# Performance work log

Hardware: AMD Instinct MI355X
Metric: run time of the kernel (lower is better)

## Reference

```python
import jax, jax.numpy as jnp
import numpy as np

N_NODES = 100000
N_EDGES = 600000
N_GRAPHS = 64
EPS = 1e-5


def setup_inputs() -> dict:
    key = jax.random.key(0)
    ks = jax.random.split(key, 8)
    x = jax.random.normal(ks[0], (N_NODES, 128), dtype=jnp.float32)
    edge_index = jax.random.randint(ks[1], (2, N_EDGES), 0, N_NODES, dtype=jnp.int64)
    batch = jnp.sort(jax.random.randint(ks[2], (N_NODES,), 0, N_GRAPHS, dtype=jnp.int64))
    conv_w = jax.random.normal(ks[3], (6, 128, 128), dtype=jnp.float32) * (1.0 / np.sqrt(128))
    conv_b = jnp.zeros((6, 128), dtype=jnp.float32)
    bn_g = jnp.ones((6, 128), dtype=jnp.float32)
    bn_b = jnp.zeros((6, 128), dtype=jnp.float32)
    lin1_w = jax.random.normal(ks[4], (128, 64), dtype=jnp.float32) * (1.0 / np.sqrt(128))
    lin1_b = jnp.zeros((64,), dtype=jnp.float32)
    lin2_w = jax.random.normal(ks[5], (64, 4), dtype=jnp.float32) * (1.0 / np.sqrt(64))
    lin2_b = jnp.zeros((4,), dtype=jnp.float32)
    return {"x": x, "edge_index": edge_index, "batch": batch,
            "conv_w": conv_w, "conv_b": conv_b, "bn_g": bn_g, "bn_b": bn_b,
            "lin1_w": lin1_w, "lin1_b": lin1_b, "lin2_w": lin2_w, "lin2_b": lin2_b}


def reference(x, edge_index, batch, conv_w, conv_b, bn_g, bn_b, lin1_w, lin1_b, lin2_w, lin2_b):
    src, dst = edge_index[0], edge_index[1]  # messages flow src -> dst (PyG source_to_target)
    n = x.shape[0]
    h = x
    # 6 stacked GCNConv(normalize=False) -> ReLU -> BatchNorm1d (training-mode batch stats)
    for i in range(6):
        m = h @ conv_w[i]                                   # [N, H] transform first
        agg = jax.ops.segment_sum(m[src], dst, num_segments=n) + conv_b[i]
        h = jax.nn.relu(agg)
        mean = h.mean(axis=0)
        var = h.var(axis=0)                                  # biased, matches torch BN
        h = (h - mean) * jax.lax.rsqrt(var + EPS) * bn_g[i] + bn_b[i]
    # global mean pool over graphs
    s = jax.ops.segment_sum(h, batch, num_segments=N_GRAPHS)          # [G, H]
    cnt = jax.ops.segment_sum(jnp.ones((n,), h.dtype), batch, num_segments=N_GRAPHS)
    pooled = s / jnp.maximum(cnt, 1.0)[:, None]
    out = pooled @ lin1_w + lin1_b
    out = out @ lin2_w + lin2_b
    return jax.nn.log_softmax(out, axis=-1)
```

## Files before the change

kernel.cpp:

```cpp
#include <hip/hip_runtime.h>
#include <math.h>

#define NN 100000
#define NE 600000
#define NG 64
#define HD 128
#define NL 6
#define NB 1563
#define PSL 16
#define ASTR 136
#define CASTB 12500

typedef unsigned short ushort_t;
typedef short short8 __attribute__((ext_vector_type(8)));
typedef float floatx4 __attribute__((ext_vector_type(4)));

__device__ __forceinline__ float bf2f(ushort_t u) {
    return __uint_as_float(((unsigned)u) << 16);
}
__device__ __forceinline__ ushort_t f2bf(float f) {
    unsigned u = __float_as_uint(f);
    unsigned r = (u + 0x7fffu + ((u >> 16) & 1u)) >> 16;
    return (ushort_t)r;
}


__global__ __launch_bounds__(256) void k_prep(const float* __restrict__ x,
                                              ushort_t* __restrict__ xb,
                                              const float* __restrict__ W,
                                              ushort_t* __restrict__ Wt,
                                              ushort_t* __restrict__ hb0,
                                              ushort_t* __restrict__ hb1) {
    if (blockIdx.x < CASTB) {
        int i = blockIdx.x * 256 + threadIdx.x;
        float4 v = ((const float4*)x)[i];
        ((ushort4*)xb)[i] = make_ushort4(f2bf(v.x), f2bf(v.y), f2bf(v.z), f2bf(v.w));
    } else {
        const float* Wl = W + (size_t)(blockIdx.x - CASTB) * 16384;
        ushort_t* Wtl = Wt + (size_t)(blockIdx.x - CASTB) * 16384;
        for (int id = threadIdx.x; id < 16384; id += 256) {
            int k = id >> 7, c = id & 127;
            Wtl[c * 128 + k] = f2bf(Wl[id]);
        }
        if (blockIdx.x == CASTB && threadIdx.x < 96) {
            int t = threadIdx.x;
            ushort_t* base = (t < 32) ? xb : ((t < 64) ? hb0 : hb1);
            *(ushort4*)(base + (size_t)NN * 128 + (size_t)(t & 31) * 4) =
                make_ushort4(0, 0, 0, 0);
        }
    }
}


__global__ __launch_bounds__(256) void k_hist(const int* __restrict__ ei, int* __restrict__ counts) {
    int e = blockIdx.x * 256 + threadIdx.x;
    if (e < NE) atomicAdd(&counts[ei[NE + e]], 1);
}

__global__ __launch_bounds__(256) void k_scan1(const int* __restrict__ counts, int* __restrict__ bsums) {
    __shared__ int s[256];
    int i = blockIdx.x * 256 + threadIdx.x;
    s[threadIdx.x] = (i < NN) ? counts[i] : 0;
    __syncthreads();
    for (int off = 128; off > 0; off >>= 1) {
        if (threadIdx.x < off) s[threadIdx.x] += s[threadIdx.x + off];
        __syncthreads();
    }
    if (threadIdx.x == 0) bsums[blockIdx.x] = s[0];
}

__global__ __launch_bounds__(256) void k_scan3m(const int* __restrict__ counts,
                                                const int* __restrict__ bsums,
                                                int* __restrict__ rowptr) {
    __shared__ int s[256];
    int t = threadIdx.x;
    int i = blockIdx.x * 256 + t;
    int v = (i < NN) ? counts[i] : 0;
    s[t] = v;
    __syncthreads();
    for (int off = 1; off < 256; off <<= 1) {
        int u = (t >= off) ? s[t - off] : 0;
        __syncthreads();
        s[t] += u;
        __syncthreads();
    }
    int incl = s[t];
    int pb = 0;
    for (int j = t; j < blockIdx.x; j += 256) pb += bsums[j];
    __syncthreads();
    s[t] = pb;
    __syncthreads();
    for (int off = 128; off > 0; off >>= 1) {
        if (t < off) s[t] += s[t + off];
        __syncthreads();
    }
    int base = s[0];
    if (i < NN) rowptr[i] = base + incl - v;
    if (i == 0) rowptr[NN] = NE;
}

__global__ __launch_bounds__(256) void k_filldh(const int* __restrict__ ei,
                                                const int* __restrict__ rowptr,
                                                int* __restrict__ cursor,
                                                int* __restrict__ colsrc,
                                                int* __restrict__ dcount,
                                                int ebl) {
    int t = threadIdx.x;
    if ((int)blockIdx.x < ebl) {
        int e = blockIdx.x * 256 + t;
        if (e < NE) {
            int d = ei[NE + e];
            int pos = rowptr[d] + atomicAdd(&cursor[d], 1);
            colsrc[pos] = ei[e];
        }
    } else {
        __shared__ int lc[64];
        if (t < 64) lc[t] = 0;
        __syncthreads();
        int n = (blockIdx.x - ebl) * 256 + t;
        if (n < NN) {
            int d = rowptr[n + 1] - rowptr[n];
            atomicAdd(&lc[min(d, 63)], 1);
        }
        __syncthreads();
        if (t < 64 && lc[t] > 0) atomicAdd(&dcount[t], lc[t]);
    }
}

__global__ __launch_bounds__(256) void k_dfill2(const int* __restrict__ rowptr,
                                                const int* __restrict__ dcount,
                                                int* __restrict__ dcursor,
                                                int* __restrict__ perm) {
    __shared__ int lc[64], lbase[64], doffs[64];
    int t = threadIdx.x;
    if (t < 64) {
        lc[t] = 0;
        int s = 0;
        for (int b = t + 1; b < 64; ++b) s += dcount[b];
        doffs[t] = s;
    }
    __syncthreads();
    int n = blockIdx.x * 256 + t;
    int b = 0, my = 0;
    if (n < NN) {
        int d = rowptr[n + 1] - rowptr[n];
        b = min(d, 63);
        my = atomicAdd(&lc[b], 1);
    }
    __syncthreads();
    if (t < 64 && lc[t] > 0) lbase[t] = atomicAdd(&dcursor[t], lc[t]);
    __syncthreads();
    if (n < NN) perm[doffs[b] + lbase[b] + my] = n;
}


__global__ __launch_bounds__(256, 4) void k_gconv(
    const ushort_t* __restrict__ hin, const int* __restrict__ perm,
    const int* __restrict__ rowptr, const int* __restrict__ colsrc,
    const float* __restrict__ stats, const float* __restrict__ bng,
    const float* __restrict__ bnb,
    const ushort_t* __restrict__ Wt, const float* __restrict__ bias,
    ushort_t* __restrict__ hout, float* __restrict__ partials) {
    __shared__ ushort_t Ab[64 * ASTR];
    __shared__ float sstat[256];
    int t = threadIdx.x;
    sstat[t] = 0.f;
    int wave = t >> 6, lane = t & 63;
    int l15 = lane & 15, quad = lane >> 4;
    int l5 = lane & 31, half = lane >> 5;
    int rowbase = blockIdx.x * 64 + wave * 16;

    int idxg = rowbase + l15;
    bool vr = idxg < NN;
    int prm = vr ? perm[idxg] : 0;
    int rb = vr ? rowptr[prm] : 0;
    int re = vr ? rowptr[prm + 1] : 0;
    int dg = re - rb;

    int f0 = l5 * 4;
    float sc[4] = {1.f, 1.f, 1.f, 1.f}, sh[4] = {0.f, 0.f, 0.f, 0.f};
    if (stats != nullptr) {
        const float inv_n = 1.0f / (float)NN;
        float4 s1 = *(const float4*)&stats[f0];
        float4 s2 = *(const float4*)&stats[HD + f0];
        float4 g4 = *(const float4*)&bng[f0];
        float4 b4 = *(const float4*)&bnb[f0];
        float m, var;
        m = s1.x * inv_n; var = fmaf(-m, m, s2.x * inv_n);
        sc[0] = g4.x * rsqrtf(var + 1e-5f); sh[0] = b4.x - m * sc[0];
        m = s1.y * inv_n; var = fmaf(-m, m, s2.y * inv_n);
        sc[1] = g4.y * rsqrtf(var + 1e-5f); sh[1] = b4.y - m * sc[1];
        m = s1.z * inv_n; var = fmaf(-m, m, s2.z * inv_n);
        sc[2] = g4.z * rsqrtf(var + 1e-5f); sh[2] = b4.z - m * sc[2];
        m = s1.w * inv_n; var = fmaf(-m, m, s2.w * inv_n);
        sc[3] = g4.w * rsqrtf(var + 1e-5f); sh[3] = b4.w - m * sc[3];
    }

    const uint2* hbl = (const uint2*)hin + l5;

    int b0 = __shfl(rb, half, 64);
    int d0 = __shfl(dg, half, 64);
    int b1 = __shfl(rb, 2 + half, 64);
    int d1 = __shfl(dg, 2 + half, 64);
    int cs0[4], cs1[4];
    #pragma unroll
    for (int eo = 0; eo < 4; ++eo) {
        int c0 = colsrc[b0 + eo];
        int c1 = colsrc[b1 + eo];
        cs0[eo] = (eo < d0) ? c0 : NN;
        cs1[eo] = (eo < d1) ? c1 : NN;
    }

    #pragma unroll 1
    for (int g = 0; g < 4; ++g) {
        int mx = max(d0, d1);
        mx = max(mx, __shfl_xor(mx, 32, 64));

        float a0[4] = {0.f, 0.f, 0.f, 0.f};
        float a1[4] = {0.f, 0.f, 0.f, 0.f};

        #pragma unroll 1
        for (int e = 0; e < mx; e += 4) {
            uint2 hv0[4], hv1[4];
            #pragma unroll
            for (int eo = 0; eo < 4; ++eo) hv0[eo] = hbl[(size_t)cs0[eo] * 32];
            #pragma unroll
            for (int eo = 0; eo < 4; ++eo) hv1[eo] = hbl[(size_t)cs1[eo] * 32];
            int nc0[4], nc1[4];
            #pragma unroll
            for (int eo = 0; eo < 4; ++eo) {
                int e4 = e + 4 + eo;
                int c0 = colsrc[b0 + e4];
                int c1 = colsrc[b1 + e4];
                nc0[eo] = (e4 < d0) ? c0 : NN;
                nc1[eo] = (e4 < d1) ? c1 : NN;
            }
            #pragma unroll
            for (int eo = 0; eo < 4; ++eo) {
                unsigned wx = hv0[eo].x, wy = hv0[eo].y;
                a0[0] += __uint_as_float(wx << 16);
                a0[1] += __uint_as_float(wx & 0xffff0000u);
                a0[2] += __uint_as_float(wy << 16);
                a0[3] += __uint_as_float(wy & 0xffff0000u);
                unsigned zx = hv1[eo].x, zy = hv1[eo].y;
                a1[0] += __uint_as_float(zx << 16);
                a1[1] += __uint_as_float(zx & 0xffff0000u);
                a1[2] += __uint_as_float(zy << 16);
                a1[3] += __uint_as_float(zy & 0xffff0000u);
            }
            #pragma unroll
            for (int eo = 0; eo < 4; ++eo) { cs0[eo] = nc0[eo]; cs1[eo] = nc1[eo]; }
        }

        int nb0 = 0, nd0 = 0, nb1 = 0, nd1 = 0;
        if (g < 3) {
            int t0 = (g + 1) * 4 + half, t1 = t0 + 2;
            nb0 = __shfl(rb, t0, 64);
            nd0 = __shfl(dg, t0, 64);
            nb1 = __shfl(rb, t1, 64);
            nd1 = __shfl(dg, t1, 64);
            #pragma unroll
            for (int eo = 0; eo < 4; ++eo) {
                int c0 = colsrc[nb0 + eo];
                int c1 = colsrc[nb1 + eo];
                cs0[eo] = (eo < nd0) ? c0 : NN;
                cs1[eo] = (eo < nd1) ? c1 : NN;
            }
        }

        float df0 = (float)d0, df1 = (float)d1;
        ushort4 u0, u1;
        u0.x = f2bf(fmaf(sc[0], a0[0], df0 * sh[0]));
        u0.y = f2bf(fmaf(sc[1], a0[1], df0 * sh[1]));
        u0.z = f2bf(fmaf(sc[2], a0[2], df0 * sh[2]));
        u0.w = f2bf(fmaf(sc[3], a0[3], df0 * sh[3]));
        u1.x = f2bf(fmaf(sc[0], a1[0], df1 * sh[0]));
        u1.y = f2bf(fmaf(sc[1], a1[1], df1 * sh[1]));
        u1.z = f2bf(fmaf(sc[2], a1[2], df1 * sh[2]));
        u1.w = f2bf(fmaf(sc[3], a1[3], df1 * sh[3]));
        *(ushort4*)&Ab[(wave * 16 + g * 4 + half) * ASTR + f0] = u0;
        *(ushort4*)&Ab[(wave * 16 + g * 4 + 2 + half) * ASTR + f0] = u1;

        b0 = nb0; d0 = nd0; b1 = nb1; d1 = nd1;
    }
    __syncthreads();

    short8 afrag[4];
    #pragma unroll
    for (int s = 0; s < 4; ++s)
        afrag[s] = *(const short8*)&Ab[(wave * 16 + l15) * ASTR + quad * 8 + s * 32];

    floatx4 acc[8];
    #pragma unroll
    for (int c = 0; c < 8; ++c) acc[c] = (floatx4){0.f, 0.f, 0.f, 0.f};
    #pragma unroll
    for (int c = 0; c < 8; ++c) {
        size_t boff = (size_t)(16 * c + l15) * 128 + quad * 8;
        #pragma unroll
        for (int s = 0; s < 4; ++s) {
            short8 bf = *(const short8*)(Wt + boff + 32 * s);
            acc[c] = __builtin_amdgcn_mfma_f32_16x16x32_bf16(afrag[s], bf, acc[c], 0, 0, 0);
        }
    }

    int orow0 = rowbase + quad * 4;
    #pragma unroll
    for (int c = 0; c < 8; ++c) {
        int col = 16 * c + l15;
        float bv = bias[col];
        float ls = 0.f, lq = 0.f;
        #pragma unroll
        for (int i = 0; i < 4; ++i) {
            float v = fmaxf(acc[c][i] + bv, 0.f);
            ushort_t bb = f2bf(v);
            Ab[(wave * 16 + quad * 4 + i) * ASTR + col] = bb;
            if (orow0 + i < NN) {
                float vr2 = bf2f(bb);
                ls += vr2;
                lq = fmaf(vr2, vr2, lq);
            }
        }
        ls += __shfl_xor(ls, 16, 64);
        ls += __shfl_xor(ls, 32, 64);
        lq += __shfl_xor(lq, 16, 64);
        lq += __shfl_xor(lq, 32, 64);
        if (quad == 0) {
            atomicAdd(&sstat[col], ls);
            atomicAdd(&sstat[128 + col], lq);
        }
    }

    #pragma unroll
    for (int it = 0; it < 4; ++it) {
        int pr = __shfl(prm, it * 4 + quad, 64);
        int ridx = rowbase + it * 4 + quad;
        if (ridx < NN) {
            short8 v = *(const short8*)&Ab[(wave * 16 + it * 4 + quad) * ASTR + l15 * 8];
            *(short8*)(hout + (size_t)pr * 128 + l15 * 8) = v;
        }
    }

    __syncthreads();
    partials[(size_t)blockIdx.x * 256 + t] = sstat[t];
}


__global__ __launch_bounds__(256) void k_red(const float* __restrict__ partials,
                                             float* __restrict__ stats) {
    int t = threadIdx.x;
    float s = 0.f;
    for (int r = blockIdx.x; r < NB; r += 64) s += partials[(size_t)r * 256 + t];
    atomicAdd(&stats[t], s);
}


__device__ __forceinline__ int lowerb(const int* __restrict__ b, int n, int key) {
    int lo = 0, hi = n;
    while (lo < hi) {
        int mid = (lo + hi) >> 1;
        if (b[mid] < key) lo = mid + 1;
        else hi = mid;
    }
    return lo;
}

__global__ __launch_bounds__(256) void k_pool1(
    const ushort_t* __restrict__ h, const int* __restrict__ batch,
    float* __restrict__ ppart) {
    int g = blockIdx.x >> 4;
    int sl = blockIdx.x & (PSL - 1);
    int lo = lowerb(batch, NN, g);
    int hi = lowerb(batch, NN, g + 1);
    int cnt = hi - lo;
    int a = lo + (int)(((long long)cnt * sl) >> 4);
    int b = lo + (int)(((long long)cnt * (sl + 1)) >> 4);
    int wave = threadIdx.x >> 6, lane = threadIdx.x & 63;
    const ushort2* h2 = (const ushort2*)h;
    float ax = 0.f, ay = 0.f;
    for (int n = a + wave; n < b; n += 4) {
        ushort2 v = h2[(size_t)n * 64 + lane];
        ax += bf2f(v.x);
        ay += bf2f(v.y);
    }
    __shared__ float2 red[4][64];
    red[wave][lane] = make_float2(ax, ay);
    __syncthreads();
    if (wave == 0) {
        float sx = 0.f, sy = 0.f;
        for (int w = 0; w < 4; ++w) {
            sx += red[w][lane].x;
            sy += red[w][lane].y;
        }
        ((float2*)ppart)[(size_t)blockIdx.x * 64 + lane] = make_float2(sx, sy);
    }
}


__global__ __launch_bounds__(64) void k_tail(
    const float* __restrict__ ppart, const int* __restrict__ batch,
    const float* __restrict__ stats, const float* __restrict__ bng, const float* __restrict__ bnb,
    const float* __restrict__ w1, const float* __restrict__ b1,
    const float* __restrict__ w2, const float* __restrict__ b2,
    float* __restrict__ out) {
    __shared__ float p[128];
    int g = blockIdx.x;
    int lane = threadIdx.x;
    float sx = 0.f, sy = 0.f;
    #pragma unroll
    for (int s = 0; s < PSL; ++s) {
        float2 v = ((const float2*)ppart)[(size_t)(g * PSL + s) * 64 + lane];
        sx += v.x;
        sy += v.y;
    }
    int cnt = lowerb(batch, NN, g + 1) - lowerb(batch, NN, g);
    int c0 = lane * 2;
    const float inv_n = 1.0f / (float)NN;
    float m0 = stats[c0] * inv_n, m1 = stats[c0 + 1] * inv_n;
    float var0 = fmaf(-m0, m0, stats[HD + c0] * inv_n);
    float var1 = fmaf(-m1, m1, stats[HD + c0 + 1] * inv_n);
    float sc0 = bng[c0] * rsqrtf(var0 + 1e-5f);
    float sc1 = bng[c0 + 1] * rsqrtf(var1 + 1e-5f);
    float sh0 = bnb[c0] - m0 * sc0;
    float sh1 = bnb[c0 + 1] - m1 * sc1;
    float denom = fmaxf((float)cnt, 1.f);
    p[c0] = (sc0 * sx + (float)cnt * sh0) / denom;
    p[c0 + 1] = (sc1 * sy + (float)cnt * sh1) / denom;
    __syncthreads();

    float hid = b1[lane];
    #pragma unroll 8
    for (int k = 0; k < 128; ++k) hid = fmaf(p[k], w1[k * 64 + lane], hid);
    float o[4];
    #pragma unroll
    for (int c = 0; c < 4; ++c) {
        float v = hid * w2[lane * 4 + c];
        #pragma unroll
        for (int off = 1; off < 64; off <<= 1) v += __shfl_xor(v, off, 64);
        o[c] = v + b2[c];
    }
    if (lane == 0) {
        float mx = fmaxf(fmaxf(o[0], o[1]), fmaxf(o[2], o[3]));
        float se = expf(o[0] - mx) + expf(o[1] - mx) + expf(o[2] - mx) + expf(o[3] - mx);
        float ls = mx + logf(se);
        #pragma unroll
        for (int c = 0; c < 4; ++c) out[g * 4 + c] = o[c] - ls;
    }
}

extern "C" void kernel_launch(void* const* d_in, const int* in_sizes, int n_in,
                              void* d_out, int out_size, void* d_ws, size_t ws_size,
                              hipStream_t stream) {
    const float* x = (const float*)d_in[0];
    const int* ei = (const int*)d_in[1];
    const int* batch = (const int*)d_in[2];
    const float* conv_w = (const float*)d_in[3];
    const float* conv_b = (const float*)d_in[4];
    const float* bn_g = (const float*)d_in[5];
    const float* bn_b = (const float*)d_in[6];
    const float* l1w = (const float*)d_in[7];
    const float* l1b = (const float*)d_in[8];
    const float* l2w = (const float*)d_in[9];
    const float* l2b = (const float*)d_in[10];
    float* out = (float*)d_out;
    (void)in_sizes; (void)n_in; (void)out_size; (void)ws_size;

    char* ws = (char*)d_ws;
    int* counts = (int*)(ws + 0);
    int* cursor = (int*)(ws + 400000);
    int* perm = (int*)(ws + 400000);
    float* stats = (float*)(ws + 800000);
    int* dcount = (int*)(ws + 806144);
    int* dcursor = (int*)(ws + 806400);
    const size_t zero_bytes = 806656;
    int* rowptr = (int*)(ws + 806656);
    int* bsums = (int*)(ws + 1206664);
    int* colsrc = (int*)(ws + 1208256);
    float* ppart = (float*)(ws + 3609280);
    float* partials = (float*)(ws + 4133568);
    ushort_t* xb = (ushort_t*)(ws + 5734144);
    ushort_t* hb0 = (ushort_t*)(ws + 31334400);
    ushort_t* hb1 = (ushort_t*)(ws + 56934656);
    ushort_t* wtbuf = (ushort_t*)(ws + 82534912);

    hipMemsetAsync(ws, 0, zero_bytes, stream);

    k_prep<<<CASTB + NL, 256, 0, stream>>>(x, xb, conv_w, wtbuf, hb0, hb1);

    int ebl = (NE + 255) / 256;
    int nb1 = (NN + 255) / 256;
    k_hist<<<ebl, 256, 0, stream>>>(ei, counts);
    k_scan1<<<nb1, 256, 0, stream>>>(counts, bsums);
    k_scan3m<<<nb1, 256, 0, stream>>>(counts, bsums, rowptr);
    k_filldh<<<ebl + nb1, 256, 0, stream>>>(ei, rowptr, cursor, colsrc, dcount, ebl);
    k_dfill2<<<nb1, 256, 0, stream>>>(rowptr, dcount, dcursor, perm);

    ushort_t* hb[2] = {hb0, hb1};
    for (int L = 0; L < NL; ++L) {
        const ushort_t* hin = (L == 0) ? xb : hb[(L + 1) & 1];
        ushort_t* hout = hb[L & 1];
        const float* lstats = (L == 0) ? nullptr : (stats + (L - 1) * 256);
        const float* lg = (L == 0) ? nullptr : (bn_g + (L - 1) * 128);
        const float* lb = (L == 0) ? nullptr : (bn_b + (L - 1) * 128);
        k_gconv<<<NB, 256, 0, stream>>>(hin, perm, rowptr, colsrc, lstats, lg, lb,
                                        wtbuf + L * 16384, conv_b + L * 128,
                                        hout, partials);
        k_red<<<64, 256, 0, stream>>>(partials, stats + L * 256);
    }
    k_pool1<<<NG * PSL, 256, 0, stream>>>(hb1, batch, ppart);
    k_tail<<<NG, 64, 0, stream>>>(ppart, batch, stats + 5 * 256, bn_g + 5 * 128, bn_b + 5 * 128,
                                  l1w, l1b, l2w, l2b, out);
}
```

Measured before the change: 646.0 us.

## Replace BN stat partials+reduce kernel with fixed-point 64-bit atomics; fuse hist into prep

Each conv block now adds its per-channel sum and sum-of-squares directly into global 64-bit fixed-point accumulators with integer atomics. This removes the partials buffer and the separate reduction kernel launched after every layer. The edge histogram is folded into the prep kernel to save another launch, and gconv launch bounds are raised to 8 blocks per CU. Fixed-point scaling keeps the summation order-independent and deterministic. It may lose precision, and the conversion to an unsigned 64-bit integer wraps negative channel sums, so correctness depends on those sums never being negative.

New measurement: 811.7 us. +25.6%, slower.

```diff
diff --git a/kernel.cpp b/kernel.cpp
--- a/kernel.cpp
+++ b/kernel.cpp
@@ -10,8 +10,12 @@
 #define PSL 16
 #define ASTR 136
 #define CASTB 12500
+#define EBL 2344
+#define FXP 1048576.0f
+#define FXI (1.0f / 1048576.0f)
 
 typedef unsigned short ushort_t;
+typedef unsigned long long ull_t;
 typedef short short8 __attribute__((ext_vector_type(8)));
 typedef float floatx4 __attribute__((ext_vector_type(4)));
 
@@ -30,32 +34,33 @@
                                               const float* __restrict__ W,
                                               ushort_t* __restrict__ Wt,
                                               ushort_t* __restrict__ hb0,
-                                              ushort_t* __restrict__ hb1) {
-    if (blockIdx.x < CASTB) {
-        int i = blockIdx.x * 256 + threadIdx.x;
+                                              ushort_t* __restrict__ hb1,
+                                              const int* __restrict__ ei,
+                                              int* __restrict__ counts) {
+    int bid = blockIdx.x;
+    if (bid < CASTB) {
+        int i = bid * 256 + threadIdx.x;
         float4 v = ((const float4*)x)[i];
         ((ushort4*)xb)[i] = make_ushort4(f2bf(v.x), f2bf(v.y), f2bf(v.z), f2bf(v.w));
-    } else {
-        const float* Wl = W + (size_t)(blockIdx.x - CASTB) * 16384;
-        ushort_t* Wtl = Wt + (size_t)(blockIdx.x - CASTB) * 16384;
+    } else if (bid < CASTB + NL) {
+        const float* Wl = W + (size_t)(bid - CASTB) * 16384;
+        ushort_t* Wtl = Wt + (size_t)(bid - CASTB) * 16384;
         for (int id = threadIdx.x; id < 16384; id += 256) {
             int k = id >> 7, c = id & 127;
             Wtl[c * 128 + k] = f2bf(Wl[id]);
         }
-        if (blockIdx.x == CASTB && threadIdx.x < 96) {
+        if (bid == CASTB && threadIdx.x < 96) {
             int t = threadIdx.x;
             ushort_t* base = (t < 32) ? xb : ((t < 64) ? hb0 : hb1);
             *(ushort4*)(base + (size_t)NN * 128 + (size_t)(t & 31) * 4) =
                 make_ushort4(0, 0, 0, 0);
         }
-    }
-}
-
-
-__global__ __launch_bounds__(256) void k_hist(const int* __restrict__ ei, int* __restrict__ counts) {
-    int e = blockIdx.x * 256 + threadIdx.x;
-    if (e < NE) atomicAdd(&counts[ei[NE + e]], 1);
-}
+    } else {
+        int e = (bid - CASTB - NL) * 256 + threadIdx.x;
+        if (e < NE) atomicAdd(&counts[ei[NE + e]], 1);
+    }
+}
+
 
 __global__ __launch_bounds__(256) void k_scan1(const int* __restrict__ counts, int* __restrict__ bsums) {
     __shared__ int s[256];
@@ -154,13 +159,13 @@
 }
 
 
-__global__ __launch_bounds__(256, 4) void k_gconv(
+__global__ __launch_bounds__(256, 8) void k_gconv(
     const ushort_t* __restrict__ hin, const int* __restrict__ perm,
     const int* __restrict__ rowptr, const int* __restrict__ colsrc,
-    const float* __restrict__ stats, const float* __restrict__ bng,
+    const ull_t* __restrict__ stats_in, const float* __restrict__ bng,
     const float* __restrict__ bnb,
     const ushort_t* __restrict__ Wt, const float* __restrict__ bias,
-    ushort_t* __restrict__ hout, float* __restrict__ partials) {
+    ushort_t* __restrict__ hout, ull_t* __restrict__ stats_out) {
     __shared__ ushort_t Ab[64 * ASTR];
     __shared__ float sstat[256];
     int t = threadIdx.x;
@@ -179,21 +184,17 @@
 
     int f0 = l5 * 4;
     float sc[4] = {1.f, 1.f, 1.f, 1.f}, sh[4] = {0.f, 0.f, 0.f, 0.f};
-    if (stats != nullptr) {
+    if (stats_in != nullptr) {
         const float inv_n = 1.0f / (float)NN;
-        float4 s1 = *(const float4*)&stats[f0];
-        float4 s2 = *(const float4*)&stats[HD + f0];
-        float4 g4 = *(const float4*)&bng[f0];
-        float4 b4 = *(const float4*)&bnb[f0];
-        float m, var;
-        m = s1.x * inv_n; var = fmaf(-m, m, s2.x * inv_n);
-        sc[0] = g4.x * rsqrtf(var + 1e-5f); sh[0] = b4.x - m * sc[0];
-        m = s1.y * inv_n; var = fmaf(-m, m, s2.y * inv_n);
-        sc[1] = g4.y * rsqrtf(var + 1e-5f); sh[1] = b4.y - m * sc[1];
-        m = s1.z * inv_n; var = fmaf(-m, m, s2.z * inv_n);
-        sc[2] = g4.z * rsqrtf(var + 1e-5f); sh[2] = b4.z - m * sc[2];
-        m = s1.w * inv_n; var = fmaf(-m, m, s2.w * inv_n);
-        sc[3] = g4.w * rsqrtf(var + 1e-5f); sh[3] = b4.w - m * sc[3];
+        #pragma unroll
+        for (int j = 0; j < 4; ++j) {
+            float s1 = (float)stats_in[f0 + j] * FXI;
+            float s2 = (float)stats_in[HD + f0 + j] * FXI;
+            float m = s1 * inv_n;
+            float var = fmaf(-m, m, s2 * inv_n);
+            sc[j] = bng[f0 + j] * rsqrtf(var + 1e-5f);
+            sh[j] = bnb[f0 + j] - m * sc[j];
+        }
     }
 
     const uint2* hbl = (const uint2*)hin + l5;
@@ -341,16 +342,7 @@
     }
 
     __syncthreads();
-    partials[(size_t)blockIdx.x * 256 + t] = sstat[t];
-}
-
-
-__global__ __launch_bounds__(256) void k_red(const float* __restrict__ partials,
-                                             float* __restrict__ stats) {
-    int t = threadIdx.x;
-    float s = 0.f;
-    for (int r = blockIdx.x; r < NB; r += 64) s += partials[(size_t)r * 256 + t];
-    atomicAdd(&stats[t], s);
+    atomicAdd(&stats_out[t], (ull_t)(sstat[t] * FXP + 0.5f));
 }
 
 
@@ -398,7 +390,7 @@
 
 __global__ __launch_bounds__(64) void k_tail(
     const float* __restrict__ ppart, const int* __restrict__ batch,
-    const float* __restrict__ stats, const float* __restrict__ bng, const float* __restrict__ bnb,
+    const ull_t* __restrict__ stats, const float* __restrict__ bng, const float* __restrict__ bnb,
     const float* __restrict__ w1, const float* __restrict__ b1,
     const float* __restrict__ w2, const float* __restrict__ b2,
     float* __restrict__ out) {
@@ -415,9 +407,12 @@
     int cnt = lowerb(batch, NN, g + 1) - lowerb(batch, NN, g);
     int c0 = lane * 2;
     const float inv_n = 1.0f / (float)NN;
-    float m0 = stats[c0] * inv_n, m1 = stats[c0 + 1] * inv_n;
-    float var0 = fmaf(-m0, m0, stats[HD + c0] * inv_n);
-    float var1 = fmaf(-m1, m1, stats[HD + c0 + 1] * inv_n);
+    float m0 = (float)stats[c0] * FXI * inv_n;
+    float m1 = (float)stats[c0 + 1] * FXI * inv_n;
+    float q0 = (float)stats[HD + c0] * FXI * inv_n;
+    float q1 = (float)stats[HD + c0 + 1] * FXI * inv_n;
+    float var0 = fmaf(-m0, m0, q0);
+    float var1 = fmaf(-m1, m1, q1);
     float sc0 = bng[c0] * rsqrtf(var0 + 1e-5f);
     float sc1 = bng[c0 + 1] * rsqrtf(var1 + 1e-5f);
     float sh0 = bnb[c0] - m0 * sc0;
@@ -468,45 +463,41 @@
     int* counts = (int*)(ws + 0);
     int* cursor = (int*)(ws + 400000);
     int* perm = (int*)(ws + 400000);
-    float* stats = (float*)(ws + 800000);
-    int* dcount = (int*)(ws + 806144);
-    int* dcursor = (int*)(ws + 806400);
-    const size_t zero_bytes = 806656;
-    int* rowptr = (int*)(ws + 806656);
-    int* bsums = (int*)(ws + 1206664);
-    int* colsrc = (int*)(ws + 1208256);
-    float* ppart = (float*)(ws + 3609280);
-    float* partials = (float*)(ws + 4133568);
-    ushort_t* xb = (ushort_t*)(ws + 5734144);
-    ushort_t* hb0 = (ushort_t*)(ws + 31334400);
-    ushort_t* hb1 = (ushort_t*)(ws + 56934656);
-    ushort_t* wtbuf = (ushort_t*)(ws + 82534912);
+    ull_t* stats64 = (ull_t*)(ws + 800000);
+    int* dcount = (int*)(ws + 812288);
+    int* dcursor = (int*)(ws + 812544);
+    const size_t zero_bytes = 812800;
+    int* rowptr = (int*)(ws + 812800);
+    int* bsums = (int*)(ws + 1212808);
+    int* colsrc = (int*)(ws + 1214400);
+    float* ppart = (float*)(ws + 3615424);
+    ushort_t* xb = (ushort_t*)(ws + 4139712);
+    ushort_t* hb0 = (ushort_t*)(ws + 29739968);
+    ushort_t* hb1 = (ushort_t*)(ws + 55340224);
+    ushort_t* wtbuf = (ushort_t*)(ws + 80940480);
 
     hipMemsetAsync(ws, 0, zero_bytes, stream);
 
-    k_prep<<<CASTB + NL, 256, 0, stream>>>(x, xb, conv_w, wtbuf, hb0, hb1);
-
-    int ebl = (NE + 255) / 256;
+    k_prep<<<CASTB + NL + EBL, 256, 0, stream>>>(x, xb, conv_w, wtbuf, hb0, hb1, ei, counts);
+
     int nb1 = (NN + 255) / 256;
-    k_hist<<<ebl, 256, 0, stream>>>(ei, counts);
     k_scan1<<<nb1, 256, 0, stream>>>(counts, bsums);
     k_scan3m<<<nb1, 256, 0, stream>>>(counts, bsums, rowptr);
-    k_filldh<<<ebl + nb1, 256, 0, stream>>>(ei, rowptr, cursor, colsrc, dcount, ebl);
+    k_filldh<<<EBL + nb1, 256, 0, stream>>>(ei, rowptr, cursor, colsrc, dcount, EBL);
     k_dfill2<<<nb1, 256, 0, stream>>>(rowptr, dcount, dcursor, perm);
 
     ushort_t* hb[2] = {hb0, hb1};
     for (int L = 0; L < NL; ++L) {
         const ushort_t* hin = (L == 0) ? xb : hb[(L + 1) & 1];
         ushort_t* hout = hb[L & 1];
-        const float* lstats = (L == 0) ? nullptr : (stats + (L - 1) * 256);
+        const ull_t* lstats = (L == 0) ? nullptr : (stats64 + (L - 1) * 256);
         const float* lg = (L == 0) ? nullptr : (bn_g + (L - 1) * 128);
         const float* lb = (L == 0) ? nullptr : (bn_b + (L - 1) * 128);
         k_gconv<<<NB, 256, 0, stream>>>(hin, perm, rowptr, colsrc, lstats, lg, lb,
                                         wtbuf + L * 16384, conv_b + L * 128,
-                                        hout, partials);
-        k_red<<<64, 256, 0, stream>>>(partials, stats + L * 256);
+                                        hout, stats64 + L * 256);
     }
     k_pool1<<<NG * PSL, 256, 0, stream>>>(hb1, batch, ppart);
-    k_tail<<<NG, 64, 0, stream>>>(ppart, batch, stats + 5 * 256, bn_g + 5 * 128, bn_b + 5 * 128,
+    k_tail<<<NG, 64, 0, stream>>>(ppart, batch, stats64 + 5 * 256, bn_g + 5 * 128, bn_b + 5 * 128,
                                   l1w, l1b, l2w, l2b, out);
 }
```
